# Kernel tuning notes

Hardware: AMD Instinct MI355X
Metric: run time of the kernel (lower is better)

Reference implementation:

```python
import jax, jax.numpy as jnp
import numpy as np

H = 16          # n_heads
DN = 128        # qk_nope_head_dim
DR = 64         # qk_rope_head_dim
DV = 128        # v_head_dim
R = 512         # kv_lora_rank
DIM = 2048
THETA = 10000.0
EPS = 1e-6
SCALE = (DN + DR) ** -0.5


def rms_norm(x, w):
    var = jnp.mean(x * x, axis=-1, keepdims=True)
    return x * jax.lax.rsqrt(var + EPS) * w


def rope_cos_sin(seqlen):
    # DeepSeek freqs: 1/theta^(2i/d) over adjacent pairs
    inv = 1.0 / (THETA ** (jnp.arange(0, DR, 2, dtype=jnp.float32) / DR))  # [DR/2]
    ang = jnp.arange(seqlen, dtype=jnp.float32)[:, None] * inv             # [s, DR/2]
    return jnp.cos(ang), jnp.sin(ang)


def apply_rope(t, cos, sin):
    # t: [b, s, h, DR]; rotate adjacent pairs (complex multiply)
    b, s, h, d = t.shape
    t = t.reshape(b, s, h, d // 2, 2)
    x0, x1 = t[..., 0], t[..., 1]
    c = cos[None, :, None, :]
    sn = sin[None, :, None, :]
    out = jnp.stack([x0 * c - x1 * sn, x0 * sn + x1 * c], axis=-1)
    return out.reshape(b, s, h, d)


def setup_inputs() -> dict:
    key = jax.random.key(0)
    ks = jax.random.split(key, 6)
    b, s = 2, 2048
    sc = lambda n: n ** -0.5
    return {
        "x": jax.random.normal(ks[0], (b, s, DIM), jnp.float32),
        "wq": jax.random.normal(ks[1], (DIM, H * (DN + DR)), jnp.float32) * sc(DIM),
        "wkv_a": jax.random.normal(ks[2], (DIM, R + DR), jnp.float32) * sc(DIM),
        "kv_norm_w": jnp.ones((R,), jnp.float32),
        "wkv_b": jax.random.normal(ks[3], (R, H * (DN + DV)), jnp.float32) * sc(R),
        "wo": jax.random.normal(ks[4], (H * DV, DIM), jnp.float32) * sc(H * DV),
    }


def reference(x, wq, wkv_a, kv_norm_w, wkv_b, wo):
    b, s, _ = x.shape
    cos, sin = rope_cos_sin(s)

    # Query projection (q_lora_rank == 0 -> direct)
    q = (x @ wq).reshape(b, s, H, DN + DR)
    q_nope, q_pe = q[..., :DN], q[..., DN:]
    q_pe = apply_rope(q_pe, cos, sin)

    # Compressed KV + decoupled rope key
    kv_a = x @ wkv_a                      # [b, s, R+DR]
    kv, k_pe = kv_a[..., :R], kv_a[..., R:]
    k_pe = apply_rope(k_pe[:, :, None, :], cos, sin)  # [b, s, 1, DR]
    kv = rms_norm(kv, kv_norm_w)
    kvb = (kv @ wkv_b).reshape(b, s, H, DN + DV)
    k_nope, v = kvb[..., :DN], kvb[..., DN:]

    qf = jnp.concatenate([q_nope, q_pe], axis=-1)                         # [b,s,H,192]
    kf = jnp.concatenate([k_nope, jnp.broadcast_to(k_pe, (b, s, H, DR))], axis=-1)

    scores = jnp.einsum("bshd,bthd->bhst", qf, kf) * SCALE
    mask = jnp.tril(jnp.ones((s, s), bool))
    scores = jnp.where(mask[None, None], scores, jnp.finfo(scores.dtype).min)
    p = jax.nn.softmax(scores, axis=-1)
    out = jnp.einsum("bhst,bthd->bshd", p, v).reshape(b, s, H * DV)
    return out @ wo
```

## Files before the change

### kernel.cpp

```cpp
#include <hip/hip_runtime.h>
#include <hip/hip_bf16.h>
#include <math.h>

#define NB 2
#define NS 2048
#define ND 2048
#define NH 16
#define DNOPE 128
#define DROPE 64
#define DVAL 128
#define RANK 512
#define QW (NH*(DNOPE+DROPE))
#define AW (RANK+DROPE)
#define AWPAD 640
#define BW (NH*(DNOPE+DVAL))
#define OW (NH*DVAL)
#define ATT_SCALE 0.07216878364870322f
#define ATT_SCALE2 0.10411758590510176f

typedef __attribute__((ext_vector_type(8))) short short8;
typedef __attribute__((ext_vector_type(4))) float f32x4;

__device__ __forceinline__ float b2f(unsigned short u) {
  unsigned x = ((unsigned)u) << 16; float f; __builtin_memcpy(&f, &x, 4); return f;
}
__device__ __forceinline__ unsigned short f2b(float f) {
  unsigned x; __builtin_memcpy(&x, &f, 4);
  unsigned r = (x + 0x7fffu + ((x >> 16) & 1u)) >> 16;
  return (unsigned short)r;
}
__device__ __forceinline__ unsigned cvtpk(float a, float b) {
  unsigned r;
  asm("v_cvt_pk_bf16_f32 %0, %1, %2" : "=v"(r) : "v"(a), "v"(b));
  return r;
}
__device__ __forceinline__ void gload16(const void* g, void* lds) {
  __builtin_amdgcn_global_load_lds((const __attribute__((address_space(1))) void*)g,
                                   (__attribute__((address_space(3))) void*)lds, 16, 0, 0);
}

__global__ __launch_bounds__(256) void k_cvt(const float* __restrict__ X,
                                             unsigned short* __restrict__ Y) {
  long i = ((long)blockIdx.x * 256 + threadIdx.x) * 4;
  float4 v = *(const float4*)(X + i);
  ushort4 o;
  o.x = f2b(v.x); o.y = f2b(v.y); o.z = f2b(v.z); o.w = f2b(v.w);
  *(ushort4*)(Y + i) = o;
}

__global__ __launch_bounds__(256) void k_transpose(const float* __restrict__ W,
                                                   unsigned short* __restrict__ WT,
                                                   int K, int N) {
  __shared__ float t[32][33];
  const int k0 = blockIdx.x * 32, n0 = blockIdx.y * 32;
  const int tx = threadIdx.x & 31, ty = threadIdx.x >> 5;
  #pragma unroll
  for (int i = 0; i < 32; i += 8) {
    int n = n0 + tx;
    float v = (n < N) ? W[(size_t)(k0 + ty + i) * N + n] : 0.f;
    t[ty + i][tx] = v;
  }
  __syncthreads();
  #pragma unroll
  for (int i = 0; i < 32; i += 8)
    WT[(size_t)(n0 + ty + i) * K + k0 + tx] = f2b(t[tx][ty + i]);
}

template <typename OutT>
__global__ __launch_bounds__(256) void gemm_bf16(
    const unsigned short* __restrict__ A, const unsigned short* __restrict__ BT,
    OutT* __restrict__ C, int M, int N, int K, int lda) {
  __shared__ short8 AsV[1024];
  __shared__ short8 BsV[1024];
  const int tid = threadIdx.x;
  const int l = tid & 63, w = tid >> 6;
  const int nwg = gridDim.x * gridDim.y;
  const int bid = blockIdx.y * gridDim.x + blockIdx.x;
  const int sbid = (bid & 7) * (nwg >> 3) + (bid >> 3);
  const int bx = sbid % gridDim.x, by = sbid / gridDim.x;
  const int bm = by * 128, bn = bx * 128;
  const int wm = (w >> 1) * 64, wn = (w & 1) * 64;
  f32x4 acc[4][4] = {};

  const int srow = tid >> 3;
  const int gk   = ((((tid & 7) * 16) ^ ((srow & 7) << 4)) >> 1);
  const int sw   = l & 7;

  for (int k0 = 0; k0 < K; k0 += 64) {
    #pragma unroll
    for (int i = 0; i < 4; ++i) {
      const int row = i * 32 + srow;
      gload16(A + (size_t)(bm + row) * lda + k0 + gk, (char*)AsV + i * 4096 + w * 1024);
      gload16(BT + (size_t)(bn + row) * K   + k0 + gk, (char*)BsV + i * 4096 + w * 1024);
    }
    __syncthreads();
    #pragma unroll
    for (int kk2 = 0; kk2 < 2; ++kk2) {
      const int kb = kk2 * 4 + (l >> 4);
      short8 af[4], bg[4];
      #pragma unroll
      for (int mi = 0; mi < 4; ++mi)
        af[mi] = AsV[(wm + mi * 16 + (l & 15)) * 8 + (kb ^ sw)];
      #pragma unroll
      for (int ni = 0; ni < 4; ++ni)
        bg[ni] = BsV[(wn + ni * 16 + (l & 15)) * 8 + (kb ^ sw)];
      #pragma unroll
      for (int mi = 0; mi < 4; ++mi)
        #pragma unroll
        for (int ni = 0; ni < 4; ++ni)
          acc[mi][ni] = __builtin_amdgcn_mfma_f32_16x16x32_bf16(af[mi], bg[ni], acc[mi][ni], 0, 0, 0);
    }
    __syncthreads();
  }

  const int r0 = bm + wm + (l >> 4) * 4;
  const int c0 = bn + wn + (l & 15);
  #pragma unroll
  for (int mi = 0; mi < 4; ++mi)
    #pragma unroll
    for (int ni = 0; ni < 4; ++ni) {
      const int col = c0 + ni * 16;
      if (col < N) {
        #pragma unroll
        for (int j = 0; j < 4; ++j) {
          float v = acc[mi][ni][j];
          if constexpr (__is_same(OutT, float))
            C[(size_t)(r0 + mi * 16 + j) * N + col] = v;
          else
            C[(size_t)(r0 + mi * 16 + j) * N + col] = f2b(v);
        }
      }
    }
}

__global__ __launch_bounds__(256) void k_rms_b(unsigned short* __restrict__ kva,
                                               const float* __restrict__ w) {
  const int row = blockIdx.x;
  unsigned short* p = kva + (long)row * AW;
  __shared__ float sd[256];
  float ss = 0.f;
  for (int j = threadIdx.x; j < RANK; j += 256) { float v = b2f(p[j]); ss += v * v; }
  sd[threadIdx.x] = ss;
  __syncthreads();
  for (int st = 128; st > 0; st >>= 1) {
    if (threadIdx.x < st) sd[threadIdx.x] += sd[threadIdx.x + st];
    __syncthreads();
  }
  const float sc = rsqrtf(sd[0] / (float)RANK + 1e-6f);
  for (int j = threadIdx.x; j < RANK; j += 256) p[j] = f2b(b2f(p[j]) * sc * w[j]);
}

__global__ __launch_bounds__(64) void k_ropek_b(unsigned short* __restrict__ kva) {
  const int row = blockIdx.x;
  const int t = row & (NS - 1);
  const int i = threadIdx.x;
  if (i >= 32) return;
  const double invf = pow(10000.0, -(double)i / 32.0);
  const double ang = (double)t * invf;
  const float c = (float)cos(ang), s = (float)sin(ang);
  unsigned short* p = kva + (long)row * AW + RANK + 2 * i;
  const float x0 = b2f(p[0]), x1 = b2f(p[1]);
  p[0] = f2b(x0 * c - x1 * s);
  p[1] = f2b(x0 * s + x1 * c);
}

__global__ __launch_bounds__(512) void k_ropeq_b(unsigned short* __restrict__ q) {
  const int row = blockIdx.x;
  const int t = row & (NS - 1);
  const int h = threadIdx.x >> 5;
  const int i = threadIdx.x & 31;
  const double invf = pow(10000.0, -(double)i / 32.0);
  const double ang = (double)t * invf;
  const float c = (float)cos(ang), s = (float)sin(ang);
  unsigned short* p = q + (long)row * QW + h * (DNOPE + DROPE) + DNOPE + 2 * i;
  const float x0 = b2f(p[0]), x1 = b2f(p[1]);
  p[0] = f2b(x0 * c - x1 * s);
  p[1] = f2b(x0 * s + x1 * c);
}

#define KBLK 64
#define KSL 24
#define VTS 72
#define PLS 72
#define QTILES (NS/128)
__global__ __launch_bounds__(512) void k_attn_mfma(
    const unsigned short* __restrict__ qg,
    const unsigned short* __restrict__ kvbg,
    const unsigned short* __restrict__ kvag,
    unsigned short* __restrict__ attg) {
  __shared__ short8 Ks[KBLK * KSL];
  __shared__ __align__(16) unsigned short VT[DVAL * VTS];
  __shared__ __align__(16) unsigned short Pl[128 * PLS];
  const int tid = threadIdx.x;
  const int l = tid & 63, w = tid >> 6;
  const int g = l >> 4, r16 = l & 15;
  const int h = blockIdx.y;
  const int b = blockIdx.z;
  const unsigned short* q   = qg   + (size_t)b * NS * QW;
  const unsigned short* kvb = kvbg + (size_t)b * NS * BW;
  const unsigned short* kva = kvag + (size_t)b * NS * AW;
  unsigned short* att = attg + (size_t)b * NS * OW;

  const unsigned short* kbs[3]; int kstp[3]; char* kdst[3];
  #pragma unroll
  for (int i = 0; i < 3; ++i) {
    const int chunk = i * 512 + tid;
    const int row = chunk / KSL, p = chunk % KSL;
    const int s = (p & ~7) | ((p & 7) ^ (row & 7));
    const int d0 = s * 8;
    if (d0 < DNOPE) { kbs[i] = kvb + (size_t)row * BW + h * 256 + d0; kstp[i] = KBLK * BW; }
    else            { kbs[i] = kva + (size_t)row * AW + RANK + (d0 - DNOPE); kstp[i] = KBLK * AW; }
    kdst[i] = (char*)Ks + (size_t)(i * 512 + (tid & ~63)) * 16;
  }
  const int vt_t = tid >> 3, vqd = tid & 7;
  const unsigned short* vbs = kvb + (size_t)vt_t * BW + h * 256 + DNOPE + vqd * 8;
  unsigned short* vwd = VT + (vqd * 8) * VTS + (vt_t ^ (vqd << 3));

  #pragma unroll 1
  for (int phase = 0; phase < 2; ++phase) {
    const int qt = phase ? (QTILES - 1 - (int)blockIdx.x) : (int)blockIdx.x;
    const int nt = 2 * qt + 2;
    const int qrow0 = qt * 128 + w * 16;

    short8 aq[6];
    {
      const unsigned short* qp = q + (size_t)(qrow0 + r16) * QW + h * 192 + g * 8;
      #pragma unroll
      for (int f = 0; f < 6; ++f) aq[f] = *(const short8*)(qp + f * 32);
    }
    f32x4 o[8] = {};
    float m_j[4], l_j[4];
    #pragma unroll
    for (int j = 0; j < 4; ++j) { m_j[j] = -1e30f; l_j[j] = 0.f; }

    const unsigned short* kq0 = kbs[0];
    const unsigned short* kq1 = kbs[1];
    const unsigned short* kq2 = kbs[2];
    const unsigned short* vq  = vbs;

    for (int kt = 0; kt < nt; ++kt) {
      gload16(kq0, kdst[0]); kq0 += kstp[0];
      gload16(kq1, kdst[1]); kq1 += kstp[1];
      gload16(kq2, kdst[2]); kq2 += kstp[2];
      #pragma unroll
      for (int pass = 0; pass < 2; ++pass) {
        short8 v = *(const short8*)(vq + pass * 64);
        unsigned short* base = vwd + pass * 64 * VTS;
        #pragma unroll
        for (int jj = 0; jj < 8; ++jj)
          base[jj * VTS] = (unsigned short)v[jj];
      }
      vq += KBLK * BW;
      __syncthreads();

      f32x4 sa[4] = {};
      __builtin_amdgcn_s_setprio(1);
      #pragma unroll
      for (int f = 0; f < 6; ++f) {
        #pragma unroll
        for (int n = 0; n < 4; ++n) {
          const int row = n * 16 + r16;
          const int s = f * 4 + g;
          const int phys = (s & ~7) | ((s & 7) ^ (row & 7));
          short8 bg = Ks[row * KSL + phys];
          sa[n] = __builtin_amdgcn_mfma_f32_16x16x32_bf16(aq[f], bg, sa[n], 0, 0, 0);
        }
      }
      __builtin_amdgcn_s_setprio(0);

      const bool diag = (kt >= nt - 2);
      float pj[4][4];
      #pragma unroll
      for (int n = 0; n < 4; ++n) {
        const int key = kt * KBLK + n * 16 + r16;
        #pragma unroll
        for (int j = 0; j < 4; ++j) {
          float v = sa[n][j] * ATT_SCALE2;
          if (diag && key > (qrow0 + g * 4 + j)) v = -1e30f;
          pj[n][j] = v;
        }
      }
      float mx4[4];
      float needf = 0.f;
      #pragma unroll
      for (int j = 0; j < 4; ++j) {
        float mx = fmaxf(fmaxf(pj[0][j], pj[1][j]), fmaxf(pj[2][j], pj[3][j]));
        #pragma unroll
        for (int o2 = 1; o2 < 16; o2 <<= 1) mx = fmaxf(mx, __shfl_xor(mx, o2, 64));
        mx4[j] = mx;
        needf += (mx > m_j[j] + 8.f) ? 1.f : 0.f;
      }
      const bool need = __any(needf > 0.f);
      #pragma unroll
      for (int j = 0; j < 4; ++j) {
        if (need) {
          const float mn = fmaxf(m_j[j], mx4[j]);
          const float c = exp2f(m_j[j] - mn);
          l_j[j] *= c;
          #pragma unroll
          for (int n8 = 0; n8 < 8; ++n8) o[n8][j] *= c;
          m_j[j] = mn;
        }
        float rs = 0.f;
        #pragma unroll
        for (int n = 0; n < 4; ++n) {
          float p = exp2f(pj[n][j] - m_j[j]);
          pj[n][j] = p;
          rs += p;
        }
        #pragma unroll
        for (int o2 = 1; o2 < 16; o2 <<= 1) rs += __shfl_xor(rs, o2, 64);
        l_j[j] += rs;
        const int prow = w * 16 + g * 4 + j;
        const unsigned pk01 = cvtpk(pj[0][j], pj[1][j]);
        const unsigned pk23 = cvtpk(pj[2][j], pj[3][j]);
        Pl[prow * PLS +  0 + r16] = (unsigned short)pk01;
        Pl[prow * PLS + 16 + r16] = (unsigned short)(pk01 >> 16);
        Pl[prow * PLS + 32 + r16] = (unsigned short)pk23;
        Pl[prow * PLS + 48 + r16] = (unsigned short)(pk23 >> 16);
      }

      const int hb = r16 >> 3;
      #pragma unroll
      for (int kk = 0; kk < 2; ++kk) {
        short8 pa = *(const short8*)&Pl[(w * 16 + r16) * PLS + kk * 32 + g * 8];
        __builtin_amdgcn_s_setprio(1);
        #pragma unroll
        for (int n8 = 0; n8 < 8; ++n8) {
          const int blk = (kk * 4 + g) ^ ((n8 * 2 + hb) & 7);
          short8 vb = *(const short8*)&VT[(n8 * 16 + r16) * VTS + blk * 8];
          o[n8] = __builtin_amdgcn_mfma_f32_16x16x32_bf16(pa, vb, o[n8], 0, 0, 0);
        }
        __builtin_amdgcn_s_setprio(0);
      }
      __syncthreads();
    }

    #pragma unroll
    for (int j = 0; j < 4; ++j) {
      const float inv = 1.0f / l_j[j];
      const size_t rowoff = (size_t)(qrow0 + g * 4 + j) * OW + h * DVAL;
      #pragma unroll
      for (int n8 = 0; n8 < 8; ++n8)
        att[rowoff + n8 * 16 + r16] = f2b(o[n8][j] * inv);
    }
  }
}

extern "C" void kernel_launch(void* const* d_in, const int* in_sizes, int n_in,
                              void* d_out, int out_size, void* d_ws, size_t ws_size,
                              hipStream_t stream) {
  const float* x      = (const float*)d_in[0];
  const float* wq     = (const float*)d_in[1];
  const float* wkv_a  = (const float*)d_in[2];
  const float* w_norm = (const float*)d_in[3];
  const float* wkv_b  = (const float*)d_in[4];
  const float* wo     = (const float*)d_in[5];
  float* out = (float*)d_out;

  unsigned short* wqT   = (unsigned short*)d_ws;
  unsigned short* wkvaT = wqT   + (long)QW * ND;
  unsigned short* wkvbT = wkvaT + (long)AWPAD * ND;
  unsigned short* woT   = wkvbT + (long)BW * RANK;
  unsigned short* xb2   = woT   + (long)ND * OW;
  unsigned short* q2    = xb2   + (long)NB * NS * ND;
  unsigned short* kva2  = q2    + (long)NB * NS * QW;
  unsigned short* kvb2  = kva2  + (long)NB * NS * AW;
  unsigned short* att2  = xb2;

  k_transpose<<<dim3(ND / 32, QW / 32),    dim3(256), 0, stream>>>(wq,    wqT,   ND,  QW);
  k_transpose<<<dim3(ND / 32, AWPAD / 32), dim3(256), 0, stream>>>(wkv_a, wkvaT, ND,  AW);
  k_transpose<<<dim3(RANK / 32, BW / 32),  dim3(256), 0, stream>>>(wkv_b, wkvbT, RANK, BW);
  k_transpose<<<dim3(OW / 32, ND / 32),    dim3(256), 0, stream>>>(wo,    woT,   OW,  ND);

  k_cvt<<<dim3((NB * NS * ND) / 1024), dim3(256), 0, stream>>>(x, xb2);
  gemm_bf16<unsigned short><<<dim3(QW / 128, (NB * NS) / 128), dim3(256), 0, stream>>>(
      xb2, wqT, q2, NB * NS, QW, ND, ND);
  gemm_bf16<unsigned short><<<dim3(5, (NB * NS) / 128), dim3(256), 0, stream>>>(
      xb2, wkvaT, kva2, NB * NS, AW, ND, ND);
  k_rms_b<<<dim3(NB * NS), dim3(256), 0, stream>>>(kva2, w_norm);
  k_ropek_b<<<dim3(NB * NS), dim3(64), 0, stream>>>(kva2);
  k_ropeq_b<<<dim3(NB * NS), dim3(512), 0, stream>>>(q2);
  gemm_bf16<unsigned short><<<dim3(BW / 128, (NB * NS) / 128), dim3(256), 0, stream>>>(
      kva2, wkvbT, kvb2, NB * NS, BW, RANK, AW);
  k_attn_mfma<<<dim3(8, NH, NB), dim3(512), 0, stream>>>(q2, kvb2, kva2, att2);
  gemm_bf16<float><<<dim3(ND / 128, (NB * NS) / 128), dim3(256), 0, stream>>>(
      att2, woT, out, NB * NS, ND, OW, OW);
}
```

Baseline: 352.4 us.

## Fuse Q and KV-A projections into one GEMM and double-buffer attention V tiles

After: 647.6 us. +83.8%, slower.

```diff
diff --git a/kernel.cpp b/kernel.cpp
--- a/kernel.cpp
+++ b/kernel.cpp
@@ -133,6 +133,71 @@
     }
 }
 
+__global__ __launch_bounds__(256) void gemm_fused_qkva(
+    const unsigned short* __restrict__ A, const unsigned short* __restrict__ BT,
+    unsigned short* __restrict__ Cq, unsigned short* __restrict__ Ckva, int K) {
+  __shared__ short8 AsV[1024];
+  __shared__ short8 BsV[1024];
+  const int tid = threadIdx.x;
+  const int l = tid & 63, w = tid >> 6;
+  const int nwg = gridDim.x * gridDim.y;
+  const int bid = blockIdx.y * gridDim.x + blockIdx.x;
+  const int sbid = (bid & 7) * (nwg >> 3) + (bid >> 3);
+  const int bx = sbid % gridDim.x, by = sbid / gridDim.x;
+  const int bm = by * 128, bn = bx * 128;
+  const int wm = (w >> 1) * 64, wn = (w & 1) * 64;
+  f32x4 acc[4][4] = {};
+
+  const int srow = tid >> 3;
+  const int gk   = ((((tid & 7) * 16) ^ ((srow & 7) << 4)) >> 1);
+  const int sw   = l & 7;
+
+  for (int k0 = 0; k0 < K; k0 += 64) {
+    #pragma unroll
+    for (int i = 0; i < 4; ++i) {
+      const int row = i * 32 + srow;
+      gload16(A + (size_t)(bm + row) * K + k0 + gk, (char*)AsV + i * 4096 + w * 1024);
+      gload16(BT + (size_t)(bn + row) * K + k0 + gk, (char*)BsV + i * 4096 + w * 1024);
+    }
+    __syncthreads();
+    #pragma unroll
+    for (int kk2 = 0; kk2 < 2; ++kk2) {
+      const int kb = kk2 * 4 + (l >> 4);
+      short8 af[4], bg[4];
+      #pragma unroll
+      for (int mi = 0; mi < 4; ++mi)
+        af[mi] = AsV[(wm + mi * 16 + (l & 15)) * 8 + (kb ^ sw)];
+      #pragma unroll
+      for (int ni = 0; ni < 4; ++ni)
+        bg[ni] = BsV[(wn + ni * 16 + (l & 15)) * 8 + (kb ^ sw)];
+      #pragma unroll
+      for (int mi = 0; mi < 4; ++mi)
+        #pragma unroll
+        for (int ni = 0; ni < 4; ++ni)
+          acc[mi][ni] = __builtin_amdgcn_mfma_f32_16x16x32_bf16(af[mi], bg[ni], acc[mi][ni], 0, 0, 0);
+    }
+    __syncthreads();
+  }
+
+  const int r0 = bm + wm + (l >> 4) * 4;
+  const int c0 = bn + wn + (l & 15);
+  #pragma unroll
+  for (int mi = 0; mi < 4; ++mi)
+    #pragma unroll
+    for (int ni = 0; ni < 4; ++ni) {
+      const int col = c0 + ni * 16;
+      #pragma unroll
+      for (int j = 0; j < 4; ++j) {
+        const float v = acc[mi][ni][j];
+        const int row = r0 + mi * 16 + j;
+        if (col < QW)
+          Cq[(size_t)row * QW + col] = f2b(v);
+        else if (col - QW < AW)
+          Ckva[(size_t)row * AW + (col - QW)] = f2b(v);
+      }
+    }
+}
+
 __global__ __launch_bounds__(256) void k_rms_b(unsigned short* __restrict__ kva,
                                                const float* __restrict__ w) {
   const int row = blockIdx.x;
@@ -181,15 +246,16 @@
 #define KBLK 64
 #define KSL 24
 #define VTS 72
+#define VBUF (DVAL*VTS)
 #define PLS 72
 #define QTILES (NS/128)
-__global__ __launch_bounds__(512) void k_attn_mfma(
+__global__ __launch_bounds__(512, 4) void k_attn_mfma(
     const unsigned short* __restrict__ qg,
     const unsigned short* __restrict__ kvbg,
     const unsigned short* __restrict__ kvag,
     unsigned short* __restrict__ attg) {
   __shared__ short8 Ks[KBLK * KSL];
-  __shared__ __align__(16) unsigned short VT[DVAL * VTS];
+  __shared__ __align__(16) unsigned short VT[2 * VBUF];
   __shared__ __align__(16) unsigned short Pl[128 * PLS];
   const int tid = threadIdx.x;
   const int l = tid & 63, w = tid >> 6;
@@ -238,21 +304,23 @@
     const unsigned short* kq2 = kbs[2];
     const unsigned short* vq  = vbs;
 
+    gload16(kq0, kdst[0]); kq0 += kstp[0];
+    gload16(kq1, kdst[1]); kq1 += kstp[1];
+    gload16(kq2, kdst[2]); kq2 += kstp[2];
+    {
+      short8 vA = *(const short8*)(vq);
+      short8 vB = *(const short8*)(vq + 64);
+      #pragma unroll
+      for (int jj = 0; jj < 8; ++jj) {
+        vwd[jj * VTS] = (unsigned short)vA[jj];
+        vwd[64 * VTS + jj * VTS] = (unsigned short)vB[jj];
+      }
+      vq += KBLK * BW;
+    }
+    __syncthreads();
+    int cur = 0;
+
     for (int kt = 0; kt < nt; ++kt) {
-      gload16(kq0, kdst[0]); kq0 += kstp[0];
-      gload16(kq1, kdst[1]); kq1 += kstp[1];
-      gload16(kq2, kdst[2]); kq2 += kstp[2];
-      #pragma unroll
-      for (int pass = 0; pass < 2; ++pass) {
-        short8 v = *(const short8*)(vq + pass * 64);
-        unsigned short* base = vwd + pass * 64 * VTS;
-        #pragma unroll
-        for (int jj = 0; jj < 8; ++jj)
-          base[jj * VTS] = (unsigned short)v[jj];
-      }
-      vq += KBLK * BW;
-      __syncthreads();
-
       f32x4 sa[4] = {};
       __builtin_amdgcn_s_setprio(1);
       #pragma unroll
@@ -267,6 +335,18 @@
         }
       }
       __builtin_amdgcn_s_setprio(0);
+      __syncthreads();
+
+      const bool pref = (kt + 1 < nt);
+      short8 vA, vB;
+      if (pref) {
+        gload16(kq0, kdst[0]); kq0 += kstp[0];
+        gload16(kq1, kdst[1]); kq1 += kstp[1];
+        gload16(kq2, kdst[2]); kq2 += kstp[2];
+        vA = *(const short8*)(vq);
+        vB = *(const short8*)(vq + 64);
+        vq += KBLK * BW;
+      }
 
       const bool diag = (kt >= nt - 2);
       float pj[4][4];
@@ -320,7 +400,17 @@
         Pl[prow * PLS + 48 + r16] = (unsigned short)(pk23 >> 16);
       }
 
+      if (pref) {
+        unsigned short* dst = vwd + (cur ^ 1) * VBUF;
+        #pragma unroll
+        for (int jj = 0; jj < 8; ++jj) {
+          dst[jj * VTS] = (unsigned short)vA[jj];
+          dst[64 * VTS + jj * VTS] = (unsigned short)vB[jj];
+        }
+      }
+
       const int hb = r16 >> 3;
+      const unsigned short* vbase = VT + cur * VBUF;
       #pragma unroll
       for (int kk = 0; kk < 2; ++kk) {
         short8 pa = *(const short8*)&Pl[(w * 16 + r16) * PLS + kk * 32 + g * 8];
@@ -328,12 +418,13 @@
         #pragma unroll
         for (int n8 = 0; n8 < 8; ++n8) {
           const int blk = (kk * 4 + g) ^ ((n8 * 2 + hb) & 7);
-          short8 vb = *(const short8*)&VT[(n8 * 16 + r16) * VTS + blk * 8];
+          short8 vb = *(const short8*)&vbase[(n8 * 16 + r16) * VTS + blk * 8];
           o[n8] = __builtin_amdgcn_mfma_f32_16x16x32_bf16(pa, vb, o[n8], 0, 0, 0);
         }
         __builtin_amdgcn_s_setprio(0);
       }
       __syncthreads();
+      cur ^= 1;
     }
 
     #pragma unroll
@@ -344,6 +435,7 @@
       for (int n8 = 0; n8 < 8; ++n8)
         att[rowoff + n8 * 16 + r16] = f2b(o[n8][j] * inv);
     }
+    __syncthreads();
   }
 }
 
@@ -374,10 +466,8 @@
   k_transpose<<<dim3(OW / 32, ND / 32),    dim3(256), 0, stream>>>(wo,    woT,   OW,  ND);
 
   k_cvt<<<dim3((NB * NS * ND) / 1024), dim3(256), 0, stream>>>(x, xb2);
-  gemm_bf16<unsigned short><<<dim3(QW / 128, (NB * NS) / 128), dim3(256), 0, stream>>>(
-      xb2, wqT, q2, NB * NS, QW, ND, ND);
-  gemm_bf16<unsigned short><<<dim3(5, (NB * NS) / 128), dim3(256), 0, stream>>>(
-      xb2, wkvaT, kva2, NB * NS, AW, ND, ND);
+  gemm_fused_qkva<<<dim3((QW + AWPAD) / 128, (NB * NS) / 128), dim3(256), 0, stream>>>(
+      xb2, wqT, q2, kva2, ND);
   k_rms_b<<<dim3(NB * NS), dim3(256), 0, stream>>>(kva2, w_norm);
   k_ropek_b<<<dim3(NB * NS), dim3(64), 0, stream>>>(kva2);
   k_ropeq_b<<<dim3(NB * NS), dim3(512), 0, stream>>>(q2);
```
